# Kernel optimization log

Measured on AMD Instinct MI355X. Metric: run time of the kernel, lower is better.

The kernel has to match this reference:

```python
import jax, jax.numpy as jnp
import numpy as np

N, F, S, D = 2048, 64, 512, 512


def setup_inputs() -> dict:
    key = jax.random.key(0)
    kx, kw, kbi, kbh = jax.random.split(key, 4)
    bound = 1.0 / np.sqrt(D)  # PyTorch RNN default init: U(-1/sqrt(hidden), 1/sqrt(hidden))
    x = jax.random.normal(kx, (N, F, S), dtype=jnp.float32)
    # Per-feature GRU input weights/biases stacked along feature axis.
    # Gate order matches PyTorch: [r, z, n] each of size D.
    W_ih = jax.random.uniform(kw, (F, 3 * D, S), minval=-bound, maxval=bound, dtype=jnp.float32)
    b_ih = jax.random.uniform(kbi, (F, 3 * D), minval=-bound, maxval=bound, dtype=jnp.float32)
    b_hh = jax.random.uniform(kbh, (F, 3 * D), minval=-bound, maxval=bound, dtype=jnp.float32)
    return {"x": x, "W_ih": W_ih, "b_ih": b_ih, "b_hh": b_hh}


def reference(x, W_ih, b_ih, b_hh):
    # Single GRU-cell step per feature with h0 = 0 (W_hh @ h0 vanishes).
    d = W_ih.shape[1] // 3
    # Batched grouped GEMM over features: [N,F,S] x [F,3D,S] -> [N,F,3D]
    gi = jnp.einsum('nfs,fgs->nfg', x, W_ih) + b_ih[None, :, :]
    i_r, i_z, i_n = gi[..., :d], gi[..., d:2 * d], gi[..., 2 * d:]
    b_hr, b_hz, b_hn = b_hh[:, :d], b_hh[:, d:2 * d], b_hh[:, 2 * d:]
    r = jax.nn.sigmoid(i_r + b_hr[None])
    z = jax.nn.sigmoid(i_z + b_hz[None])
    n = jnp.tanh(i_n + r * b_hn[None])
    h = (1.0 - z) * n  # h1 = (1-z)*n + z*h0, h0 = 0
    return h  # [N, F, D]
```

## Files before the change

kernel.cpp:

```cpp
#include <hip/hip_runtime.h>
#include <stdint.h>


#define NN 2048
#define FF 64
#define SS 512
#define DD 512
#define BM 128
#define BD 64
#define BK 64
#define NKT 8

#define A_SLAB 16384
#define B_SLAB 24576
#define XT_BYTES ((long)64 * 16 * 8 * A_SLAB)
#define WT_BYTES ((long)64 * 8 * 8 * B_SLAB)

typedef float f32x4 __attribute__((ext_vector_type(4)));
typedef __bf16 bf16x8 __attribute__((ext_vector_type(8)));
typedef unsigned short ushort8 __attribute__((ext_vector_type(8)));
typedef unsigned int uint32x4 __attribute__((ext_vector_type(4)));

#define AS1 __attribute__((address_space(1)))
#define AS3 __attribute__((address_space(3)))

__device__ __forceinline__ void gload16(const void* gsrc, void* ldst) {
    __builtin_amdgcn_global_load_lds(
        (const AS1 unsigned int*)(uintptr_t)gsrc,
        (AS3 unsigned int*)(unsigned int)(uintptr_t)ldst,
        16, 0, 0);
}

__device__ __forceinline__ ushort8 cvt8(const f32x4 a, const f32x4 b) {
    ushort8 r;
    r[0] = __builtin_bit_cast(unsigned short, (__bf16)a[0]);
    r[1] = __builtin_bit_cast(unsigned short, (__bf16)a[1]);
    r[2] = __builtin_bit_cast(unsigned short, (__bf16)a[2]);
    r[3] = __builtin_bit_cast(unsigned short, (__bf16)a[3]);
    r[4] = __builtin_bit_cast(unsigned short, (__bf16)b[0]);
    r[5] = __builtin_bit_cast(unsigned short, (__bf16)b[1]);
    r[6] = __builtin_bit_cast(unsigned short, (__bf16)b[2]);
    r[7] = __builtin_bit_cast(unsigned short, (__bf16)b[3]);
    return r;
}

__device__ __forceinline__ float fast_sigmoid(float v) {
    return 1.0f / (1.0f + __expf(-v));
}
__device__ __forceinline__ float fast_tanh(float v) {
    return 1.0f - 2.0f / (__expf(2.0f * v) + 1.0f);
}

extern "C" __global__ __launch_bounds__(256)
void prep_x(const float* __restrict__ x, ushort8* __restrict__ xT) {
    const int b  = blockIdx.x;
    const int f  = b >> 7;
    const int mt = (b >> 3) & 15;
    const int kt = b & 7;
    const int t  = threadIdx.x;
    const long slab = (long)b * 1024;
#pragma unroll
    for (int p = 0; p < 4; ++p) {
        int q = p * 256 + t;
        int r = q >> 3;
        int s = (q & 7) ^ (r & 7);
        const f32x4* src = (const f32x4*)(x + ((long)(mt * BM + r) * FF + f) * SS
                                          + kt * BK + s * 8);
        xT[slab + q] = cvt8(src[0], src[1]);
    }
}

extern "C" __global__ __launch_bounds__(256)
void prep_w(const float* __restrict__ W, ushort8* __restrict__ wT) {
    const int b  = blockIdx.x;
    const int f  = b >> 6;
    const int dt = (b >> 3) & 7;
    const int kt = b & 7;
    const int t  = threadIdx.x;
    const long slab = (long)b * 1536;
#pragma unroll
    for (int p = 0; p < 6; ++p) {
        int q  = p * 256 + t;
        int g  = q >> 9;
        int rr = (q >> 3) & 63;
        int s  = (q & 7) ^ (rr & 7);
        const f32x4* src = (const f32x4*)(W + ((long)f * 1536 + g * DD + dt * BD + rr) * SS
                                          + kt * BK + s * 8);
        wT[slab + q] = cvt8(src[0], src[1]);
    }
}

extern "C" __global__ __launch_bounds__(256, 3)
void gru_gemm(const unsigned char* __restrict__ xT, const unsigned char* __restrict__ wT,
              const float* __restrict__ b_ih, const float* __restrict__ b_hh,
              float* __restrict__ out)
{
    __shared__ __align__(16) unsigned char lds[40960];

    const int t     = threadIdx.x;
    const int lane  = t & 63;
    const int wid   = t >> 6;
    const int wm    = wid >> 1;
    const int wd    = wid & 1;
    const int lrow  = lane & 15;
    const int khalf = lane >> 4;

    const int bid  = blockIdx.x;
    const int xcd  = bid & 7;
    const int lid  = bid >> 3;
    const int work = xcd * 1024 + lid;
    const int f    = work >> 7;
    const int rem  = work & 127;
    const int mt   = rem >> 3;
    const int dt   = rem & 7;
    const int n0   = mt * BM;
    const int d0   = dt * BD;

    const unsigned char* aSlab = xT + (long)((f * 16 + mt) * 8) * A_SLAB;
    const unsigned char* bSlab = wT + (long)((f * 8 + dt) * 8) * B_SLAB;
    const int ldsW = (t & 192) * 16;

    f32x4 acc[3][4][2];
#pragma unroll
    for (int g = 0; g < 3; ++g)
#pragma unroll
        for (int i = 0; i < 4; ++i)
#pragma unroll
            for (int j = 0; j < 2; ++j)
                acc[g][i][j] = (f32x4){0.f, 0.f, 0.f, 0.f};

    for (int kt = 0; kt < NKT; ++kt) {
        __syncthreads();
#pragma unroll
        for (int p = 0; p < 4; ++p)
            gload16(aSlab + kt * A_SLAB + (p * 256 + t) * 16,
                    lds + p * 4096 + ldsW);
#pragma unroll
        for (int p = 0; p < 6; ++p)
            gload16(bSlab + kt * B_SLAB + (p * 256 + t) * 16,
                    lds + 16384 + p * 4096 + ldsW);
        __syncthreads();

#pragma unroll
        for (int kb = 0; kb < 2; ++kb) {
            bf16x8 af[4];
#pragma unroll
            for (int i = 0; i < 4; ++i) {
                int row = wm * 64 + i * 16 + lrow;
                int off = row * 128 + ((kb * 64 + khalf * 16) ^ ((row & 7) << 4));
                af[i] = __builtin_bit_cast(bf16x8, *(const uint32x4*)(lds + off));
            }
            bf16x8 bfr[3][2];
#pragma unroll
            for (int g = 0; g < 3; ++g)
#pragma unroll
                for (int j = 0; j < 2; ++j) {
                    int dr  = wd * 32 + j * 16 + lrow;
                    int off = 16384 + g * 8192 + dr * 128 +
                              ((kb * 64 + khalf * 16) ^ ((dr & 7) << 4));
                    bfr[g][j] = __builtin_bit_cast(bf16x8, *(const uint32x4*)(lds + off));
                }
#pragma unroll
            for (int g = 0; g < 3; ++g)
#pragma unroll
                for (int i = 0; i < 4; ++i)
#pragma unroll
                    for (int j = 0; j < 2; ++j)
                        acc[g][i][j] = __builtin_amdgcn_mfma_f32_16x16x32_bf16(
                            af[i], bfr[g][j], acc[g][i][j], 0, 0, 0);
        }
    }

    const long bBase = (long)f * (3 * DD);
#pragma unroll
    for (int j = 0; j < 2; ++j) {
        int d = d0 + wd * 32 + j * 16 + lrow;
        float bihr = b_ih[bBase + d];
        float bihz = b_ih[bBase + DD + d];
        float bihn = b_ih[bBase + 2 * DD + d];
        float bhr  = b_hh[bBase + d];
        float bhz  = b_hh[bBase + DD + d];
        float bhn  = b_hh[bBase + 2 * DD + d];
#pragma unroll
        for (int i = 0; i < 4; ++i) {
#pragma unroll
            for (int q = 0; q < 4; ++q) {
                int row = wm * 64 + i * 16 + khalf * 4 + q;
                float gr = acc[0][i][j][q] + bihr + bhr;
                float gz = acc[1][i][j][q] + bihz + bhz;
                float gy = acc[2][i][j][q] + bihn;
                float r  = fast_sigmoid(gr);
                float z  = fast_sigmoid(gz);
                float nv = fast_tanh(gy + r * bhn);
                long oi  = ((long)(n0 + row) * FF + f) * DD + d;
                out[oi]  = (1.0f - z) * nv;
            }
        }
    }
}

extern "C" __global__ __launch_bounds__(256, 3)
void gru_fused_fb(const float* __restrict__ x, const float* __restrict__ W,
                  const float* __restrict__ b_ih, const float* __restrict__ b_hh,
                  float* __restrict__ out)
{
    __shared__ __align__(16) unsigned char lds[28672];
    const int t     = threadIdx.x;
    const int lane  = t & 63;
    const int wid   = t >> 6;
    const int wm    = wid >> 1;
    const int wd    = wid & 1;
    const int lrow  = lane & 15;
    const int khalf = lane >> 4;
    const int bid  = blockIdx.x;
    const int xcd  = bid & 7;
    const int lid  = bid >> 3;
    const int work = xcd * 2048 + lid;
    const int f    = work >> 8;
    const int rem  = work & 255;
    const int n0   = (rem >> 4) * BM;
    const int d0   = (rem & 15) * 32;
    const int colSeg = t & 7;
    const int rBase  = t >> 3;
    const float* aPtr[4]; int aOff[4];
#pragma unroll
    for (int p = 0; p < 4; ++p) {
        int row = rBase + 32 * p;
        aPtr[p] = x + ((long)(n0 + row) * FF + f) * SS + colSeg * 8;
        aOff[p] = row * 128 + ((colSeg * 16) ^ ((row & 7) << 4));
    }
    const float* bPtr[3]; int bOff[3];
#pragma unroll
    for (int p = 0; p < 3; ++p) {
        int ra = rBase + 32 * p;
        int gate = ra >> 5, dr = ra & 31;
        bPtr[p] = W + ((long)f * 1536 + gate * DD + d0 + dr) * SS + colSeg * 8;
        bOff[p] = 16384 + gate * 4096 + dr * 128 + ((colSeg * 16) ^ ((dr & 7) << 4));
    }
    f32x4 acc[3][4];
#pragma unroll
    for (int g = 0; g < 3; ++g)
#pragma unroll
        for (int i = 0; i < 4; ++i) acc[g][i] = (f32x4){0.f, 0.f, 0.f, 0.f};
    f32x4 va[4][2], vb[3][2];
#pragma unroll
    for (int p = 0; p < 4; ++p) { const f32x4* g = (const f32x4*)aPtr[p]; va[p][0] = g[0]; va[p][1] = g[1]; }
#pragma unroll
    for (int p = 0; p < 3; ++p) { const f32x4* g = (const f32x4*)bPtr[p]; vb[p][0] = g[0]; vb[p][1] = g[1]; }
    for (int kt = 0; kt < NKT; ++kt) {
        __syncthreads();
#pragma unroll
        for (int p = 0; p < 4; ++p) *(ushort8*)(lds + aOff[p]) = cvt8(va[p][0], va[p][1]);
#pragma unroll
        for (int p = 0; p < 3; ++p) *(ushort8*)(lds + bOff[p]) = cvt8(vb[p][0], vb[p][1]);
        __syncthreads();
        if (kt + 1 < NKT) {
            const long koff = (long)(kt + 1) * BK;
#pragma unroll
            for (int p = 0; p < 4; ++p) { const f32x4* g = (const f32x4*)(aPtr[p] + koff); va[p][0] = g[0]; va[p][1] = g[1]; }
#pragma unroll
            for (int p = 0; p < 3; ++p) { const f32x4* g = (const f32x4*)(bPtr[p] + koff); vb[p][0] = g[0]; vb[p][1] = g[1]; }
        }
#pragma unroll
        for (int kb = 0; kb < 2; ++kb) {
            bf16x8 af[4];
#pragma unroll
            for (int i = 0; i < 4; ++i) {
                int row = wm * 64 + i * 16 + lrow;
                int off = row * 128 + ((kb * 64 + khalf * 16) ^ ((row & 7) << 4));
                af[i] = __builtin_bit_cast(bf16x8, *(const uint32x4*)(lds + off));
            }
            bf16x8 bfr[3];
#pragma unroll
            for (int g = 0; g < 3; ++g) {
                int dr = wd * 16 + lrow;
                int off = 16384 + g * 4096 + dr * 128 + ((kb * 64 + khalf * 16) ^ ((dr & 7) << 4));
                bfr[g] = __builtin_bit_cast(bf16x8, *(const uint32x4*)(lds + off));
            }
#pragma unroll
            for (int g = 0; g < 3; ++g)
#pragma unroll
                for (int i = 0; i < 4; ++i)
                    acc[g][i] = __builtin_amdgcn_mfma_f32_16x16x32_bf16(af[i], bfr[g], acc[g][i], 0, 0, 0);
        }
    }
    const long bBase = (long)f * 1536;
    {
        int d = d0 + wd * 16 + lrow;
        float bihr = b_ih[bBase + d], bihz = b_ih[bBase + DD + d], bihn = b_ih[bBase + 2 * DD + d];
        float bhr = b_hh[bBase + d], bhz = b_hh[bBase + DD + d], bhn = b_hh[bBase + 2 * DD + d];
#pragma unroll
        for (int i = 0; i < 4; ++i)
#pragma unroll
            for (int q = 0; q < 4; ++q) {
                int row = wm * 64 + i * 16 + khalf * 4 + q;
                float r  = fast_sigmoid(acc[0][i][q] + bihr + bhr);
                float z  = fast_sigmoid(acc[1][i][q] + bihz + bhz);
                float nv = fast_tanh(acc[2][i][q] + bihn + r * bhn);
                out[((long)(n0 + row) * FF + f) * DD + d] = (1.0f - z) * nv;
            }
    }
}

extern "C" void kernel_launch(void* const* d_in, const int* in_sizes, int n_in,
                              void* d_out, int out_size, void* d_ws, size_t ws_size,
                              hipStream_t stream) {
    const float* x   = (const float*)d_in[0];
    const float* W   = (const float*)d_in[1];
    const float* bih = (const float*)d_in[2];
    const float* bhh = (const float*)d_in[3];
    float* out       = (float*)d_out;

    if (ws_size >= (size_t)(XT_BYTES + WT_BYTES)) {
        unsigned char* xT = (unsigned char*)d_ws;
        unsigned char* wT = xT + XT_BYTES;
        prep_x<<<dim3(8192), dim3(256), 0, stream>>>(x, (ushort8*)xT);
        prep_w<<<dim3(4096), dim3(256), 0, stream>>>(W, (ushort8*)wT);
        gru_gemm<<<dim3(8192), dim3(256), 0, stream>>>(xT, wT, bih, bhh, out);
    } else {
        gru_fused_fb<<<dim3(16384), dim3(256), 0, stream>>>(x, W, bih, bhh, out);
    }
}
```

Baseline: 441.9 us.

## Double-buffer LDS loads and widen GEMM tile to 256 rows with 512 threads

The GEMM kernel now uses 512-thread blocks covering 256 rows of N, so each W tile loaded into LDS is reused across twice as many rows. It double-buffers LDS, issuing async global-to-LDS loads two k-steps ahead and waiting with explicit vmcnt counts, so loads overlap the MFMA work. MFMA sections are also raised to higher wave priority. The cost is more LDS per block (about 112KB) and fewer resident blocks, plus dependence on exact vmcnt accounting for correctness.

```diff
diff --git a/kernel.cpp b/kernel.cpp
--- a/kernel.cpp
+++ b/kernel.cpp
@@ -6,7 +6,7 @@
 #define FF 64
 #define SS 512
 #define DD 512
-#define BM 128
+#define BM 256
 #define BD 64
 #define BK 64
 #define NKT 8
@@ -15,6 +15,7 @@
 #define B_SLAB 24576
 #define XT_BYTES ((long)64 * 16 * 8 * A_SLAB)
 #define WT_BYTES ((long)64 * 8 * 8 * B_SLAB)
+#define BUF_STRIDE 57344
 
 typedef float f32x4 __attribute__((ext_vector_type(4)));
 typedef __bf16 bf16x8 __attribute__((ext_vector_type(8)));
@@ -64,7 +65,7 @@
         int q = p * 256 + t;
         int r = q >> 3;
         int s = (q & 7) ^ (r & 7);
-        const f32x4* src = (const f32x4*)(x + ((long)(mt * BM + r) * FF + f) * SS
+        const f32x4* src = (const f32x4*)(x + ((long)(mt * 128 + r) * FF + f) * SS
                                           + kt * BK + s * 8);
         xT[slab + q] = cvt8(src[0], src[1]);
     }
@@ -90,12 +91,12 @@
     }
 }
 
-extern "C" __global__ __launch_bounds__(256, 3)
+extern "C" __global__ __launch_bounds__(512, 2)
 void gru_gemm(const unsigned char* __restrict__ xT, const unsigned char* __restrict__ wT,
               const float* __restrict__ b_ih, const float* __restrict__ b_hh,
               float* __restrict__ out)
 {
-    __shared__ __align__(16) unsigned char lds[40960];
+    __shared__ __align__(16) unsigned char lds[2 * BUF_STRIDE];
 
     const int t     = threadIdx.x;
     const int lane  = t & 63;
@@ -108,17 +109,36 @@
     const int bid  = blockIdx.x;
     const int xcd  = bid & 7;
     const int lid  = bid >> 3;
-    const int work = xcd * 1024 + lid;
-    const int f    = work >> 7;
-    const int rem  = work & 127;
+    const int work = xcd * 512 + lid;
+    const int f    = work >> 6;
+    const int rem  = work & 63;
     const int mt   = rem >> 3;
     const int dt   = rem & 7;
     const int n0   = mt * BM;
     const int d0   = dt * BD;
 
-    const unsigned char* aSlab = xT + (long)((f * 16 + mt) * 8) * A_SLAB;
-    const unsigned char* bSlab = wT + (long)((f * 8 + dt) * 8) * B_SLAB;
-    const int ldsW = (t & 192) * 16;
+    const unsigned char* aS0 = xT + (long)((f * 16 + mt * 2) * 8) * A_SLAB;
+    const unsigned char* aS1 = xT + (long)((f * 16 + mt * 2 + 1) * 8) * A_SLAB;
+    const unsigned char* bS  = wT + (long)((f * 8 + dt) * 8) * B_SLAB;
+
+#define STAGE(KT)                                                              \
+    do {                                                                       \
+        unsigned char* dst = lds + ((KT) & 1) * BUF_STRIDE;                    \
+        gload16(aS0 + (long)(KT) * A_SLAB + (0 * 512 + t) * 16,                \
+                dst + (0 * 512 + t) * 16);                                     \
+        gload16(aS0 + (long)(KT) * A_SLAB + (1 * 512 + t) * 16,                \
+                dst + (1 * 512 + t) * 16);                                     \
+        gload16(aS1 + (long)(KT) * A_SLAB + (0 * 512 + t) * 16,                \
+                dst + 16384 + (0 * 512 + t) * 16);                             \
+        gload16(aS1 + (long)(KT) * A_SLAB + (1 * 512 + t) * 16,                \
+                dst + 16384 + (1 * 512 + t) * 16);                             \
+        gload16(bS + (long)(KT) * B_SLAB + (0 * 512 + t) * 16,                 \
+                dst + 32768 + (0 * 512 + t) * 16);                             \
+        gload16(bS + (long)(KT) * B_SLAB + (1 * 512 + t) * 16,                 \
+                dst + 32768 + (1 * 512 + t) * 16);                             \
+        gload16(bS + (long)(KT) * B_SLAB + (2 * 512 + t) * 16,                 \
+                dst + 32768 + (2 * 512 + t) * 16);                             \
+    } while (0)
 
     f32x4 acc[3][4][2];
 #pragma unroll
@@ -129,18 +149,18 @@
             for (int j = 0; j < 2; ++j)
                 acc[g][i][j] = (f32x4){0.f, 0.f, 0.f, 0.f};
 
+    STAGE(0);
+    STAGE(1);
+
+#pragma unroll
     for (int kt = 0; kt < NKT; ++kt) {
-        __syncthreads();
-#pragma unroll
-        for (int p = 0; p < 4; ++p)
-            gload16(aSlab + kt * A_SLAB + (p * 256 + t) * 16,
-                    lds + p * 4096 + ldsW);
-#pragma unroll
-        for (int p = 0; p < 6; ++p)
-            gload16(bSlab + kt * B_SLAB + (p * 256 + t) * 16,
-                    lds + 16384 + p * 4096 + ldsW);
-        __syncthreads();
-
+        if (kt < NKT - 1)
+            asm volatile("s_waitcnt vmcnt(7)" ::: "memory");
+        else
+            asm volatile("s_waitcnt vmcnt(0)" ::: "memory");
+        __builtin_amdgcn_s_barrier();
+
+        const unsigned char* buf = lds + (kt & 1) * BUF_STRIDE;
 #pragma unroll
         for (int kb = 0; kb < 2; ++kb) {
             bf16x8 af[4];
@@ -148,7 +168,7 @@
             for (int i = 0; i < 4; ++i) {
                 int row = wm * 64 + i * 16 + lrow;
                 int off = row * 128 + ((kb * 64 + khalf * 16) ^ ((row & 7) << 4));
-                af[i] = __builtin_bit_cast(bf16x8, *(const uint32x4*)(lds + off));
+                af[i] = __builtin_bit_cast(bf16x8, *(const uint32x4*)(buf + off));
             }
             bf16x8 bfr[3][2];
 #pragma unroll
@@ -156,10 +176,11 @@
 #pragma unroll
                 for (int j = 0; j < 2; ++j) {
                     int dr  = wd * 32 + j * 16 + lrow;
-                    int off = 16384 + g * 8192 + dr * 128 +
+                    int off = 32768 + g * 8192 + dr * 128 +
                               ((kb * 64 + khalf * 16) ^ ((dr & 7) << 4));
-                    bfr[g][j] = __builtin_bit_cast(bf16x8, *(const uint32x4*)(lds + off));
+                    bfr[g][j] = __builtin_bit_cast(bf16x8, *(const uint32x4*)(buf + off));
                 }
+            __builtin_amdgcn_s_setprio(1);
 #pragma unroll
             for (int g = 0; g < 3; ++g)
 #pragma unroll
@@ -168,7 +189,13 @@
                     for (int j = 0; j < 2; ++j)
                         acc[g][i][j] = __builtin_amdgcn_mfma_f32_16x16x32_bf16(
                             af[i], bfr[g][j], acc[g][i][j], 0, 0, 0);
+            __builtin_amdgcn_s_setprio(0);
         }
+
+        __builtin_amdgcn_s_barrier();
+        asm volatile("" ::: "memory");
+        if (kt + 2 < NKT)
+            STAGE(kt + 2);
     }
 
     const long bBase = (long)f * (3 * DD);
@@ -197,6 +224,7 @@
             }
         }
     }
+#undef STAGE
 }
 
 extern "C" __global__ __launch_bounds__(256, 3)
@@ -218,7 +246,7 @@
     const int work = xcd * 2048 + lid;
     const int f    = work >> 8;
     const int rem  = work & 255;
-    const int n0   = (rem >> 4) * BM;
+    const int n0   = (rem >> 4) * 128;
     const int d0   = (rem & 15) * 32;
     const int colSeg = t & 7;
     const int rBase  = t >> 3;
@@ -247,14 +275,14 @@
     for (int p = 0; p < 4; ++p) { const f32x4* g = (const f32x4*)aPtr[p]; va[p][0] = g[0]; va[p][1] = g[1]; }
 #pragma unroll
     for (int p = 0; p < 3; ++p) { const f32x4* g = (const f32x4*)bPtr[p]; vb[p][0] = g[0]; vb[p][1] = g[1]; }
-    for (int kt = 0; kt < NKT; ++kt) {
+    for (int kt = 0; kt < 8; ++kt) {
         __syncthreads();
 #pragma unroll
         for (int p = 0; p < 4; ++p) *(ushort8*)(lds + aOff[p]) = cvt8(va[p][0], va[p][1]);
 #pragma unroll
         for (int p = 0; p < 3; ++p) *(ushort8*)(lds + bOff[p]) = cvt8(vb[p][0], vb[p][1]);
         __syncthreads();
-        if (kt + 1 < NKT) {
+        if (kt + 1 < 8) {
             const long koff = (long)(kt + 1) * BK;
 #pragma unroll
             for (int p = 0; p < 4; ++p) { const f32x4* g = (const f32x4*)(aPtr[p] + koff); va[p][0] = g[0]; va[p][1] = g[1]; }
@@ -316,7 +344,7 @@
         unsigned char* wT = xT + XT_BYTES;
         prep_x<<<dim3(8192), dim3(256), 0, stream>>>(x, (ushort8*)xT);
         prep_w<<<dim3(4096), dim3(256), 0, stream>>>(W, (ushort8*)wT);
-        gru_gemm<<<dim3(8192), dim3(256), 0, stream>>>(xT, wT, bih, bhh, out);
+        gru_gemm<<<dim3(4096), dim3(512), 0, stream>>>(xT, wT, bih, bhh, out);
     } else {
         gru_fused_fb<<<dim3(16384), dim3(256), 0, stream>>>(x, W, bih, bhh, out);
     }
```

Result: slower. 507.0 us (+14.7%).

## Double-buffer LDS in gru_gemm with async prefetch and MFMA priority

Applied to the files above, without the earlier changes.

Replaces the single-buffer load-sync-compute loop in gru_gemm with a fully unrolled double-buffered pipeline. A tiles are prefetched one k-step ahead and B tiles two steps ahead, using manual vmcnt waits and split barriers so global-to-LDS copies overlap with MFMA work. MFMA blocks are wrapped in s_setprio to favour the math wave. LDS use doubles to 80KB and occupancy drops from 3 to 2 blocks per CU, and the hand-placed waitcnt values risk races if the counts are wrong.

```diff
diff --git a/kernel.cpp b/kernel.cpp
--- a/kernel.cpp
+++ b/kernel.cpp
@@ -6,15 +6,13 @@
 #define FF 64
 #define SS 512
 #define DD 512
-#define BM 128
-#define BD 64
-#define BK 64
 #define NKT 8
 
 #define A_SLAB 16384
 #define B_SLAB 24576
 #define XT_BYTES ((long)64 * 16 * 8 * A_SLAB)
 #define WT_BYTES ((long)64 * 8 * 8 * B_SLAB)
+#define BUFSZ 40960
 
 typedef float f32x4 __attribute__((ext_vector_type(4)));
 typedef __bf16 bf16x8 __attribute__((ext_vector_type(8)));
@@ -64,8 +62,8 @@
         int q = p * 256 + t;
         int r = q >> 3;
         int s = (q & 7) ^ (r & 7);
-        const f32x4* src = (const f32x4*)(x + ((long)(mt * BM + r) * FF + f) * SS
-                                          + kt * BK + s * 8);
+        const f32x4* src = (const f32x4*)(x + ((long)(mt * 128 + r) * FF + f) * SS
+                                          + kt * 64 + s * 8);
         xT[slab + q] = cvt8(src[0], src[1]);
     }
 }
@@ -84,18 +82,18 @@
         int g  = q >> 9;
         int rr = (q >> 3) & 63;
         int s  = (q & 7) ^ (rr & 7);
-        const f32x4* src = (const f32x4*)(W + ((long)f * 1536 + g * DD + dt * BD + rr) * SS
-                                          + kt * BK + s * 8);
+        const f32x4* src = (const f32x4*)(W + ((long)f * 1536 + g * DD + dt * 64 + rr) * SS
+                                          + kt * 64 + s * 8);
         wT[slab + q] = cvt8(src[0], src[1]);
     }
 }
 
-extern "C" __global__ __launch_bounds__(256, 3)
+extern "C" __global__ __launch_bounds__(256, 2)
 void gru_gemm(const unsigned char* __restrict__ xT, const unsigned char* __restrict__ wT,
               const float* __restrict__ b_ih, const float* __restrict__ b_hh,
               float* __restrict__ out)
 {
-    __shared__ __align__(16) unsigned char lds[40960];
+    __shared__ __align__(16) unsigned char lds[2 * BUFSZ];
 
     const int t     = threadIdx.x;
     const int lane  = t & 63;
@@ -113,8 +111,8 @@
     const int rem  = work & 127;
     const int mt   = rem >> 3;
     const int dt   = rem & 7;
-    const int n0   = mt * BM;
-    const int d0   = dt * BD;
+    const int n0   = mt * 128;
+    const int d0   = dt * 64;
 
     const unsigned char* aSlab = xT + (long)((f * 16 + mt) * 8) * A_SLAB;
     const unsigned char* bSlab = wT + (long)((f * 8 + dt) * 8) * B_SLAB;
@@ -129,47 +127,88 @@
             for (int j = 0; j < 2; ++j)
                 acc[g][i][j] = (f32x4){0.f, 0.f, 0.f, 0.f};
 
-    for (int kt = 0; kt < NKT; ++kt) {
-        __syncthreads();
-#pragma unroll
-        for (int p = 0; p < 4; ++p)
-            gload16(aSlab + kt * A_SLAB + (p * 256 + t) * 16,
-                    lds + p * 4096 + ldsW);
-#pragma unroll
-        for (int p = 0; p < 6; ++p)
-            gload16(bSlab + kt * B_SLAB + (p * 256 + t) * 16,
-                    lds + 16384 + p * 4096 + ldsW);
-        __syncthreads();
-
-#pragma unroll
-        for (int kb = 0; kb < 2; ++kb) {
-            bf16x8 af[4];
-#pragma unroll
-            for (int i = 0; i < 4; ++i) {
-                int row = wm * 64 + i * 16 + lrow;
-                int off = row * 128 + ((kb * 64 + khalf * 16) ^ ((row & 7) << 4));
-                af[i] = __builtin_bit_cast(bf16x8, *(const uint32x4*)(lds + off));
-            }
-            bf16x8 bfr[3][2];
-#pragma unroll
-            for (int g = 0; g < 3; ++g)
-#pragma unroll
-                for (int j = 0; j < 2; ++j) {
-                    int dr  = wd * 32 + j * 16 + lrow;
-                    int off = 16384 + g * 8192 + dr * 128 +
-                              ((kb * 64 + khalf * 16) ^ ((dr & 7) << 4));
-                    bfr[g][j] = __builtin_bit_cast(bf16x8, *(const uint32x4*)(lds + off));
-                }
-#pragma unroll
-            for (int g = 0; g < 3; ++g)
-#pragma unroll
-                for (int i = 0; i < 4; ++i)
-#pragma unroll
-                    for (int j = 0; j < 2; ++j)
-                        acc[g][i][j] = __builtin_amdgcn_mfma_f32_16x16x32_bf16(
-                            af[i], bfr[g][j], acc[g][i][j], 0, 0, 0);
+#pragma unroll
+    for (int p = 0; p < 4; ++p)
+        gload16(aSlab + (p * 256 + t) * 16, lds + p * 4096 + ldsW);
+#pragma unroll
+    for (int p = 0; p < 6; ++p)
+        gload16(bSlab + (p * 256 + t) * 16, lds + 16384 + p * 4096 + ldsW);
+#pragma unroll
+    for (int p = 0; p < 6; ++p)
+        gload16(bSlab + (long)B_SLAB + (p * 256 + t) * 16,
+                lds + BUFSZ + 16384 + p * 4096 + ldsW);
+
+#define LDA(DST, BUFP, KB)                                                     \
+    _Pragma("unroll")                                                          \
+    for (int i = 0; i < 4; ++i) {                                              \
+        int row = wm * 64 + i * 16 + lrow;                                     \
+        int off = row * 128 + (((KB) * 64 + khalf * 16) ^ ((row & 7) << 4));   \
+        DST[i] = __builtin_bit_cast(bf16x8, *(const uint32x4*)((BUFP) + off)); \
+    }
+
+#define LDB(DST, BUFP, KB)                                                     \
+    _Pragma("unroll")                                                          \
+    for (int g = 0; g < 3; ++g)                                                \
+        _Pragma("unroll")                                                      \
+        for (int j = 0; j < 2; ++j) {                                          \
+            int dr  = wd * 32 + j * 16 + lrow;                                 \
+            int off = 16384 + g * 8192 + dr * 128 +                            \
+                      (((KB) * 64 + khalf * 16) ^ ((dr & 7) << 4));            \
+            DST[g][j] = __builtin_bit_cast(bf16x8,                             \
+                            *(const uint32x4*)((BUFP) + off));                 \
         }
-    }
+
+#define MM(AV, BV)                                                             \
+    __builtin_amdgcn_s_setprio(1);                                             \
+    _Pragma("unroll")                                                          \
+    for (int g = 0; g < 3; ++g)                                                \
+        _Pragma("unroll")                                                      \
+        for (int i = 0; i < 4; ++i)                                            \
+            _Pragma("unroll")                                                  \
+            for (int j = 0; j < 2; ++j)                                        \
+                acc[g][i][j] = __builtin_amdgcn_mfma_f32_16x16x32_bf16(        \
+                    AV[i], BV[g][j], acc[g][i][j], 0, 0, 0);                   \
+    __builtin_amdgcn_s_setprio(0);
+
+#define ITER(KT, VM, DO_A, DO_B)                                               \
+    {                                                                          \
+        asm volatile("s_waitcnt vmcnt(" #VM ")" ::: "memory");                 \
+        __builtin_amdgcn_s_barrier();                                          \
+        asm volatile("" ::: "memory");                                         \
+        const unsigned char* bufC = lds + ((KT) & 1) * BUFSZ;                  \
+        unsigned char* bufO = lds + (((KT) & 1) ^ 1) * BUFSZ;                  \
+        bf16x8 av[4], bv0[3][2], bv1[3][2];                                    \
+        LDB(bv0, bufC, 0);                                                     \
+        LDB(bv1, bufC, 1);                                                     \
+        LDA(av, bufC, 0);                                                      \
+        MM(av, bv0);                                                           \
+        asm volatile("s_waitcnt lgkmcnt(0)" ::: "memory");                     \
+        __builtin_amdgcn_s_barrier();                                          \
+        asm volatile("" ::: "memory");                                         \
+        LDA(av, bufC, 1);                                                      \
+        if (DO_A) {                                                            \
+            _Pragma("unroll")                                                  \
+            for (int p = 0; p < 4; ++p)                                        \
+                gload16(aSlab + (long)((KT) + 1) * A_SLAB + (p * 256 + t) * 16,\
+                        bufO + p * 4096 + ldsW);                               \
+        }                                                                      \
+        if (DO_B) {                                                            \
+            _Pragma("unroll")                                                  \
+            for (int p = 0; p < 6; ++p)                                        \
+                gload16(bSlab + (long)((KT) + 2) * B_SLAB + (p * 256 + t) * 16,\
+                        (unsigned char*)bufC + 16384 + p * 4096 + ldsW);       \
+        }                                                                      \
+        MM(av, bv1);                                                           \
+    }
+
+    ITER(0, 6, 1, 1)
+    ITER(1, 6, 1, 1)
+    ITER(2, 6, 1, 1)
+    ITER(3, 6, 1, 1)
+    ITER(4, 6, 1, 1)
+    ITER(5, 6, 1, 1)
+    ITER(6, 6, 1, 0)
+    ITER(7, 0, 0, 0)
 
     const long bBase = (long)f * (3 * DD);
 #pragma unroll
@@ -197,6 +236,10 @@
             }
         }
     }
+#undef LDA
+#undef LDB
+#undef MM
+#undef ITER
 }
 
 extern "C" __global__ __launch_bounds__(256, 3)
@@ -218,7 +261,7 @@
     const int work = xcd * 2048 + lid;
     const int f    = work >> 8;
     const int rem  = work & 255;
-    const int n0   = (rem >> 4) * BM;
+    const int n0   = (rem >> 4) * 128;
     const int d0   = (rem & 15) * 32;
     const int colSeg = t & 7;
     const int rBase  = t >> 3;
@@ -247,15 +290,15 @@
     for (int p = 0; p < 4; ++p) { const f32x4* g = (const f32x4*)aPtr[p]; va[p][0] = g[0]; va[p][1] = g[1]; }
 #pragma unroll
     for (int p = 0; p < 3; ++p) { const f32x4* g = (const f32x4*)bPtr[p]; vb[p][0] = g[0]; vb[p][1] = g[1]; }
-    for (int kt = 0; kt < NKT; ++kt) {
+    for (int kt = 0; kt < 8; ++kt) {
         __syncthreads();
 #pragma unroll
         for (int p = 0; p < 4; ++p) *(ushort8*)(lds + aOff[p]) = cvt8(va[p][0], va[p][1]);
 #pragma unroll
         for (int p = 0; p < 3; ++p) *(ushort8*)(lds + bOff[p]) = cvt8(vb[p][0], vb[p][1]);
         __syncthreads();
-        if (kt + 1 < NKT) {
-            const long koff = (long)(kt + 1) * BK;
+        if (kt + 1 < 8) {
+            const long koff = (long)(kt + 1) * 64;
 #pragma unroll
             for (int p = 0; p < 4; ++p) { const f32x4* g = (const f32x4*)(aPtr[p] + koff); va[p][0] = g[0]; va[p][1] = g[1]; }
 #pragma unroll
```

Result: slower. 467.6 us (+5.8%).

## Double-buffer GEMM K-halves in LDS and merge prep kernels

Applied to the files above, without the earlier changes.

The main GEMM loop now splits each 64-wide K tile into two 32-wide halves held in two LDS regions. The next stage's async global-to-LDS loads are issued while MFMAs run on the current one, using explicit vmcnt/lgkmcnt waits, raw barriers and s_setprio. The prep layout is reorganised so two rows share a 128-byte line with an XOR swizzle matching the new fragment reads. The x and W prep kernels are merged into one launch. This is meant to hide global load latency and cut one launch, at the cost of more barriers per K step and hand-tuned waitcnt values that must match the load count.

```diff
diff --git a/kernel.cpp b/kernel.cpp
--- a/kernel.cpp
+++ b/kernel.cpp
@@ -6,15 +6,12 @@
 #define FF 64
 #define SS 512
 #define DD 512
-#define BM 128
-#define BD 64
-#define BK 64
-#define NKT 8
 
 #define A_SLAB 16384
 #define B_SLAB 24576
 #define XT_BYTES ((long)64 * 16 * 8 * A_SLAB)
 #define WT_BYTES ((long)64 * 8 * 8 * B_SLAB)
+#define REGION 20480
 
 typedef float f32x4 __attribute__((ext_vector_type(4)));
 typedef __bf16 bf16x8 __attribute__((ext_vector_type(8)));
@@ -52,41 +49,49 @@
 }
 
 extern "C" __global__ __launch_bounds__(256)
-void prep_x(const float* __restrict__ x, ushort8* __restrict__ xT) {
-    const int b  = blockIdx.x;
-    const int f  = b >> 7;
-    const int mt = (b >> 3) & 15;
-    const int kt = b & 7;
-    const int t  = threadIdx.x;
-    const long slab = (long)b * 1024;
-#pragma unroll
-    for (int p = 0; p < 4; ++p) {
-        int q = p * 256 + t;
-        int r = q >> 3;
-        int s = (q & 7) ^ (r & 7);
-        const f32x4* src = (const f32x4*)(x + ((long)(mt * BM + r) * FF + f) * SS
-                                          + kt * BK + s * 8);
-        xT[slab + q] = cvt8(src[0], src[1]);
-    }
-}
-
-extern "C" __global__ __launch_bounds__(256)
-void prep_w(const float* __restrict__ W, ushort8* __restrict__ wT) {
-    const int b  = blockIdx.x;
-    const int f  = b >> 6;
-    const int dt = (b >> 3) & 7;
-    const int kt = b & 7;
-    const int t  = threadIdx.x;
-    const long slab = (long)b * 1536;
-#pragma unroll
-    for (int p = 0; p < 6; ++p) {
-        int q  = p * 256 + t;
-        int g  = q >> 9;
-        int rr = (q >> 3) & 63;
-        int s  = (q & 7) ^ (rr & 7);
-        const f32x4* src = (const f32x4*)(W + ((long)f * 1536 + g * DD + dt * BD + rr) * SS
-                                          + kt * BK + s * 8);
-        wT[slab + q] = cvt8(src[0], src[1]);
+void prep_xw(const float* __restrict__ x, const float* __restrict__ W,
+             ushort8* __restrict__ xT, ushort8* __restrict__ wT) {
+    const int t = threadIdx.x;
+    int b = blockIdx.x;
+    if (b < 8192) {
+        const int f  = b >> 7;
+        const int mt = (b >> 3) & 15;
+        const int kt = b & 7;
+        const long slab = (long)b * 1024;
+#pragma unroll
+        for (int p = 0; p < 4; ++p) {
+            int q    = p * 256 + t;
+            int kb   = q >> 9;
+            int u    = q & 511;
+            int line = u >> 3;
+            int v    = u & 7;
+            int r    = line * 2 + (v >> 2);
+            int ks   = (v & 3) ^ (line & 3);
+            int k    = kt * 64 + kb * 32 + ks * 8;
+            const f32x4* src = (const f32x4*)(x + ((long)(mt * 128 + r) * FF + f) * SS + k);
+            xT[slab + q] = cvt8(src[0], src[1]);
+        }
+    } else {
+        b -= 8192;
+        const int f  = b >> 6;
+        const int dt = (b >> 3) & 7;
+        const int kt = b & 7;
+        const long slab = (long)b * 1536;
+#pragma unroll
+        for (int p = 0; p < 6; ++p) {
+            int q    = p * 256 + t;
+            int kb   = (q >= 768) ? 1 : 0;
+            int u    = q - kb * 768;
+            int gate = u >> 8;
+            int w    = u & 255;
+            int line = w >> 3;
+            int v    = w & 7;
+            int r    = line * 2 + (v >> 2);
+            int ks   = (v & 3) ^ (line & 3);
+            int k    = kt * 64 + kb * 32 + ks * 8;
+            const f32x4* src = (const f32x4*)(W + ((long)f * 1536 + gate * DD + dt * 64 + r) * SS + k);
+            wT[slab + q] = cvt8(src[0], src[1]);
+        }
     }
 }
 
@@ -95,7 +100,7 @@
               const float* __restrict__ b_ih, const float* __restrict__ b_hh,
               float* __restrict__ out)
 {
-    __shared__ __align__(16) unsigned char lds[40960];
+    __shared__ __align__(16) unsigned char lds[2 * REGION];
 
     const int t     = threadIdx.x;
     const int lane  = t & 63;
@@ -113,8 +118,8 @@
     const int rem  = work & 127;
     const int mt   = rem >> 3;
     const int dt   = rem & 7;
-    const int n0   = mt * BM;
-    const int d0   = dt * BD;
+    const int n0   = mt * 128;
+    const int d0   = dt * 64;
 
     const unsigned char* aSlab = xT + (long)((f * 16 + mt) * 8) * A_SLAB;
     const unsigned char* bSlab = wT + (long)((f * 8 + dt) * 8) * B_SLAB;
@@ -129,47 +134,77 @@
             for (int j = 0; j < 2; ++j)
                 acc[g][i][j] = (f32x4){0.f, 0.f, 0.f, 0.f};
 
-    for (int kt = 0; kt < NKT; ++kt) {
-        __syncthreads();
-#pragma unroll
-        for (int p = 0; p < 4; ++p)
-            gload16(aSlab + kt * A_SLAB + (p * 256 + t) * 16,
-                    lds + p * 4096 + ldsW);
-#pragma unroll
-        for (int p = 0; p < 6; ++p)
-            gload16(bSlab + kt * B_SLAB + (p * 256 + t) * 16,
-                    lds + 16384 + p * 4096 + ldsW);
-        __syncthreads();
-
-#pragma unroll
-        for (int kb = 0; kb < 2; ++kb) {
-            bf16x8 af[4];
-#pragma unroll
-            for (int i = 0; i < 4; ++i) {
-                int row = wm * 64 + i * 16 + lrow;
-                int off = row * 128 + ((kb * 64 + khalf * 16) ^ ((row & 7) << 4));
-                af[i] = __builtin_bit_cast(bf16x8, *(const uint32x4*)(lds + off));
-            }
-            bf16x8 bfr[3][2];
-#pragma unroll
-            for (int g = 0; g < 3; ++g)
-#pragma unroll
-                for (int j = 0; j < 2; ++j) {
-                    int dr  = wd * 32 + j * 16 + lrow;
-                    int off = 16384 + g * 8192 + dr * 128 +
-                              ((kb * 64 + khalf * 16) ^ ((dr & 7) << 4));
-                    bfr[g][j] = __builtin_bit_cast(bf16x8, *(const uint32x4*)(lds + off));
-                }
-#pragma unroll
-            for (int g = 0; g < 3; ++g)
-#pragma unroll
-                for (int i = 0; i < 4; ++i)
-#pragma unroll
-                    for (int j = 0; j < 2; ++j)
-                        acc[g][i][j] = __builtin_amdgcn_mfma_f32_16x16x32_bf16(
-                            af[i], bfr[g][j], acc[g][i][j], 0, 0, 0);
-        }
-    }
+#define STAGE(H)                                                               \
+    {                                                                          \
+        const unsigned char* as_ = aSlab + (long)((H) >> 1) * A_SLAB           \
+                                   + ((H) & 1) * 8192;                         \
+        const unsigned char* bs_ = bSlab + (long)((H) >> 1) * B_SLAB           \
+                                   + ((H) & 1) * 12288;                        \
+        unsigned char* rg_ = lds + ((H) & 1) * REGION;                         \
+        _Pragma("unroll")                                                      \
+        for (int p = 0; p < 2; ++p)                                            \
+            gload16(as_ + p * 4096 + t * 16, rg_ + p * 4096 + ldsW);           \
+        _Pragma("unroll")                                                      \
+        for (int p = 0; p < 3; ++p)                                            \
+            gload16(bs_ + p * 4096 + t * 16, rg_ + 8192 + p * 4096 + ldsW);    \
+    }
+
+#define ITER(H, VM, DOS)                                                       \
+    {                                                                          \
+        asm volatile("s_waitcnt vmcnt(" #VM ")" ::: "memory");                 \
+        __builtin_amdgcn_s_barrier();                                          \
+        const unsigned char* rg_ = lds + ((H) & 1) * REGION;                   \
+        bf16x8 av[4], bv[3][2];                                                \
+        _Pragma("unroll")                                                      \
+        for (int i = 0; i < 4; ++i) {                                          \
+            int row = wm * 64 + i * 16 + lrow;                                 \
+            int off = (row >> 1) * 128 + (row & 1) * 64 +                      \
+                      ((khalf ^ ((row >> 1) & 3)) << 4);                       \
+            av[i] = __builtin_bit_cast(bf16x8, *(const uint32x4*)(rg_ + off)); \
+        }                                                                      \
+        _Pragma("unroll")                                                      \
+        for (int g = 0; g < 3; ++g)                                            \
+            _Pragma("unroll")                                                  \
+            for (int j = 0; j < 2; ++j) {                                      \
+                int dr  = wd * 32 + j * 16 + lrow;                             \
+                int off = 8192 + g * 4096 + (dr >> 1) * 128 + (dr & 1) * 64 +  \
+                          ((khalf ^ ((dr >> 1) & 3)) << 4);                    \
+                bv[g][j] = __builtin_bit_cast(bf16x8,                          \
+                               *(const uint32x4*)(rg_ + off));                 \
+            }                                                                  \
+        asm volatile("s_waitcnt lgkmcnt(0)" ::: "memory");                     \
+        __builtin_amdgcn_s_barrier();                                          \
+        if (DOS) STAGE((H) + 2);                                               \
+        __builtin_amdgcn_s_setprio(1);                                         \
+        _Pragma("unroll")                                                      \
+        for (int g = 0; g < 3; ++g)                                            \
+            _Pragma("unroll")                                                  \
+            for (int i = 0; i < 4; ++i)                                        \
+                _Pragma("unroll")                                              \
+                for (int j = 0; j < 2; ++j)                                    \
+                    acc[g][i][j] = __builtin_amdgcn_mfma_f32_16x16x32_bf16(    \
+                        av[i], bv[g][j], acc[g][i][j], 0, 0, 0);               \
+        __builtin_amdgcn_s_setprio(0);                                         \
+    }
+
+    STAGE(0)
+    STAGE(1)
+    ITER(0, 5, 1)
+    ITER(1, 5, 1)
+    ITER(2, 5, 1)
+    ITER(3, 5, 1)
+    ITER(4, 5, 1)
+    ITER(5, 5, 1)
+    ITER(6, 5, 1)
+    ITER(7, 5, 1)
+    ITER(8, 5, 1)
+    ITER(9, 5, 1)
+    ITER(10, 5, 1)
+    ITER(11, 5, 1)
+    ITER(12, 5, 1)
+    ITER(13, 5, 1)
+    ITER(14, 5, 0)
+    ITER(15, 0, 0)
 
     const long bBase = (long)f * (3 * DD);
 #pragma unroll
@@ -197,6 +232,8 @@
             }
         }
     }
+#undef STAGE
+#undef ITER
 }
 
 extern "C" __global__ __launch_bounds__(256, 3)
@@ -218,7 +255,7 @@
     const int work = xcd * 2048 + lid;
     const int f    = work >> 8;
     const int rem  = work & 255;
-    const int n0   = (rem >> 4) * BM;
+    const int n0   = (rem >> 4) * 128;
     const int d0   = (rem & 15) * 32;
     const int colSeg = t & 7;
     const int rBase  = t >> 3;
@@ -247,15 +284,15 @@
     for (int p = 0; p < 4; ++p) { const f32x4* g = (const f32x4*)aPtr[p]; va[p][0] = g[0]; va[p][1] = g[1]; }
 #pragma unroll
     for (int p = 0; p < 3; ++p) { const f32x4* g = (const f32x4*)bPtr[p]; vb[p][0] = g[0]; vb[p][1] = g[1]; }
-    for (int kt = 0; kt < NKT; ++kt) {
+    for (int kt = 0; kt < 8; ++kt) {
         __syncthreads();
 #pragma unroll
         for (int p = 0; p < 4; ++p) *(ushort8*)(lds + aOff[p]) = cvt8(va[p][0], va[p][1]);
 #pragma unroll
         for (int p = 0; p < 3; ++p) *(ushort8*)(lds + bOff[p]) = cvt8(vb[p][0], vb[p][1]);
         __syncthreads();
-        if (kt + 1 < NKT) {
-            const long koff = (long)(kt + 1) * BK;
+        if (kt + 1 < 8) {
+            const long koff = (long)(kt + 1) * 64;
 #pragma unroll
             for (int p = 0; p < 4; ++p) { const f32x4* g = (const f32x4*)(aPtr[p] + koff); va[p][0] = g[0]; va[p][1] = g[1]; }
 #pragma unroll
@@ -314,8 +351,7 @@
     if (ws_size >= (size_t)(XT_BYTES + WT_BYTES)) {
         unsigned char* xT = (unsigned char*)d_ws;
         unsigned char* wT = xT + XT_BYTES;
-        prep_x<<<dim3(8192), dim3(256), 0, stream>>>(x, (ushort8*)xT);
-        prep_w<<<dim3(4096), dim3(256), 0, stream>>>(W, (ushort8*)wT);
+        prep_xw<<<dim3(12288), dim3(256), 0, stream>>>(x, W, (ushort8*)xT, (ushort8*)wT);
         gru_gemm<<<dim3(8192), dim3(256), 0, stream>>>(xT, wT, bih, bhh, out);
     } else {
         gru_fused_fb<<<dim3(16384), dim3(256), 0, stream>>>(x, W, bih, bhh, out);
```

Result: slower. 494.7 us (+11.9%).
